# Performance work log

Measured on AMD Instinct MI355X. Metric: run time of the kernel, lower is better.

The kernel has to match this reference:

```python
import jax, jax.numpy as jnp
import numpy as np

N_NODES = 50000
N_EDGES = 800000
D_FEAT = 128
N_LAYERS = 3
HALF = 64  # units // 2 per kernel in tf_geometric MeanGraphSage
HIDDEN = 256
NUM_LABELS = 40


def setup_inputs() -> dict:
    key = jax.random.key(0)
    ks = jax.random.split(key, 6)
    x = jax.random.normal(ks[0], (N_NODES, D_FEAT), dtype=jnp.float32)
    edge_index = jax.random.randint(ks[1], (2, N_EDGES), 0, N_NODES, dtype=jnp.int32)
    self_kernels = jax.random.normal(ks[2], (N_LAYERS, D_FEAT, HALF), dtype=jnp.float32) * 0.05
    neighbor_kernels = jax.random.normal(ks[3], (N_LAYERS, D_FEAT, HALF), dtype=jnp.float32) * 0.05
    biases = jnp.zeros((N_LAYERS, 2 * HALF), dtype=jnp.float32)
    mlp_w1 = jax.random.normal(ks[4], (2 * HALF, HIDDEN), dtype=jnp.float32) * 0.05
    mlp_b1 = jnp.zeros((HIDDEN,), dtype=jnp.float32)
    mlp_w2 = jax.random.normal(ks[5], (HIDDEN, NUM_LABELS), dtype=jnp.float32) * 0.05
    mlp_b2 = jnp.zeros((NUM_LABELS,), dtype=jnp.float32)
    return {"x": x, "edge_index": edge_index, "self_kernels": self_kernels,
            "neighbor_kernels": neighbor_kernels, "biases": biases,
            "mlp_w1": mlp_w1, "mlp_b1": mlp_b1, "mlp_w2": mlp_w2, "mlp_b2": mlp_b2}


def reference(x, edge_index, self_kernels, neighbor_kernels, biases,
              mlp_w1, mlp_b1, mlp_w2, mlp_b2):
    n = x.shape[0]
    row, col = edge_index[0], edge_index[1]  # row: target node, col: source node
    # in-degree counts (graph is fixed across layers)
    ones = jnp.ones((edge_index.shape[1],), dtype=x.dtype)
    deg = jax.ops.segment_sum(ones, row, num_segments=n)  # [N]
    inv_deg = (1.0 / jnp.maximum(deg, 1.0))[:, None]      # [N,1]

    h = x
    for i in range(N_LAYERS):
        # mean-neighbor aggregation: gather source feats, segment-sum to targets
        nbr_sum = jax.ops.segment_sum(h[col], row, num_segments=n)  # [N,D]
        nbr_mean = nbr_sum * inv_deg
        from_self = h @ self_kernels[i]        # [N,HALF]
        from_nbr = nbr_mean @ neighbor_kernels[i]  # [N,HALF]
        h = jax.nn.relu(jnp.concatenate([from_self, from_nbr], axis=1) + biases[i])

    # MLP head (Flatten on [N,128] is a no-op)
    h = jax.nn.relu(h @ mlp_w1 + mlp_b1)
    return h @ mlp_w2 + mlp_b2
```

## Files before the change

kernel.cpp:

```cpp
#include <hip/hip_runtime.h>
#include <hip/hip_bf16.h>
#include <hip/hip_fp16.h>
#include <cstdint>
#include <cstddef>

#define N_NODES 50000
#define N_PAD   50176
#define N_EDGES 800000
#define D_FEAT  128
#define HALF    64
#define HIDDEN  256
#define LABELS  40

#define NBUCK 196
#define BCAP  5632
#define EDGES_PER_BLK 4096

#define HID_STRIDE 264

typedef __attribute__((ext_vector_type(8))) short bf16x8;
typedef __attribute__((ext_vector_type(4))) float f32x4;

#define PK_SELF(L) ((size_t)(L) * 8192)
#define PK_NBR(L)  (24576 + (size_t)(L) * 8192)
#define PK_W1      49152
#define PK_W2      81920
#define PK_TOTAL   94208

__device__ inline uint16_t f2bf_bits(float f) {
    __hip_bfloat16 b = __float2bfloat16(f);
    uint16_t u; __builtin_memcpy(&u, &b, 2); return u;
}

__device__ inline float2 h2f(uint32_t u) {
    __half2 h; __builtin_memcpy(&h, &u, 4);
    return __half22float2(h);
}

__global__ __launch_bounds__(1024) void bucket_scatter_kernel(
        const int* __restrict__ row, const int* __restrict__ col,
        int* __restrict__ bucket_cursor, uint32_t* __restrict__ staged) {
    __shared__ int hist[NBUCK];
    __shared__ int hbase[NBUCK];
    int tid  = threadIdx.x;
    int e0   = blockIdx.x * EDGES_PER_BLK;
    int eend = e0 + EDGES_PER_BLK; if (eend > N_EDGES) eend = N_EDGES;

    for (int i = tid; i < NBUCK; i += 1024) hist[i] = 0;
    __syncthreads();

    int rr[4], cc[4]; int ne = 0;
    for (int e = e0 + tid; e < eend; e += 1024) {
        rr[ne] = row[e]; cc[ne] = col[e]; ne++;
    }
    for (int i = 0; i < ne; i++) atomicAdd(&hist[rr[i] >> 8], 1);
    __syncthreads();

    for (int i = tid; i < NBUCK; i += 1024) {
        hbase[i] = atomicAdd(&bucket_cursor[i], hist[i]);
        hist[i]  = 0;
    }
    __syncthreads();

    for (int i = 0; i < ne; i++) {
        int b   = rr[i] >> 8;
        int off = atomicAdd(&hist[b], 1);
        int pos = hbase[b] + off;
        if (pos < BCAP)
            staged[(size_t)b * BCAP + pos] =
                ((uint32_t)(rr[i] & 255) << 16) | (uint32_t)cc[i];
    }
}

__global__ __launch_bounds__(256) void pack_all_kernel(
        const float* __restrict__ selfk, const float* __restrict__ nbrk,
        const float* __restrict__ w1, const float* __restrict__ w2,
        __hip_bfloat16* __restrict__ wpack) {
    int m = blockIdx.y;
    const float* W; int K, Ncols, Npad; size_t dstoff;
    if (m < 3)      { W = selfk + (size_t)m*D_FEAT*HALF;      K=128; Ncols=64;  Npad=64;  dstoff = PK_SELF(m); }
    else if (m < 6) { W = nbrk  + (size_t)(m-3)*D_FEAT*HALF;  K=128; Ncols=64;  Npad=64;  dstoff = PK_NBR(m-3); }
    else if (m == 6){ W = w1;                                 K=128; Ncols=256; Npad=256; dstoff = PK_W1; }
    else            { W = w2;                                 K=256; Ncols=40;  Npad=48;  dstoff = PK_W2; }
    int ksteps = K / 32;
    int total  = ksteps * (Npad / 16) * 64;
    int t = blockIdx.x * blockDim.x + threadIdx.x;
    if (t >= total) return;
    int lane = t & 63;
    int rest = t >> 6;
    int ks   = rest % ksteps;
    int ns   = rest / ksteps;
    int colb = ns * 16 + (lane & 15);
    int kb   = ks * 32 + (lane >> 4) * 8;
    __hip_bfloat16* dst = wpack + dstoff + (size_t)t * 8;
#pragma unroll
    for (int j = 0; j < 8; j++) {
        float v = (colb < Ncols) ? W[(size_t)(kb + j) * Ncols + colb] : 0.f;
        dst[j] = __float2bfloat16(v);
    }
}

template<bool AF32>
__device__ inline void gemm_wave_body(
        const void* __restrict__ Ain, int row0, int lane,
        const __hip_bfloat16* __restrict__ wpack_self,
        const __hip_bfloat16* __restrict__ wpack_nbr,
        const float* __restrict__ bias,
        __hip_bfloat16* __restrict__ hout, uint16_t* __restrict__ zn) {
    int lrow = lane & 15, lgrp = lane >> 4;

    const __hip_bfloat16 *hr0 = nullptr, *hr1 = nullptr;
    const float *xr0 = nullptr, *xr1 = nullptr;
    if constexpr (AF32) {
        const float* x = (const float*)Ain;
        int r0 = min(row0 + lrow, N_NODES - 1);
        int r1 = min(row0 + lrow + 16, N_NODES - 1);
        xr0 = x + (size_t)r0 * D_FEAT + lgrp * 8;
        xr1 = x + (size_t)r1 * D_FEAT + lgrp * 8;
    } else {
        const __hip_bfloat16* h = (const __hip_bfloat16*)Ain;
        hr0 = h + (size_t)(row0 + lrow) * D_FEAT + lgrp * 8;
        hr1 = hr0 + (size_t)16 * D_FEAT;
    }

    f32x4 accS[2][4] = {};
    f32x4 accN[2][4] = {};
#pragma unroll
    for (int ks = 0; ks < 4; ks++) {
        bf16x8 a0, a1;
        if constexpr (AF32) {
            float4 u0  = *(const float4*)(xr0 + ks * 32);
            float4 u0b = *(const float4*)(xr0 + ks * 32 + 4);
            float4 u1  = *(const float4*)(xr1 + ks * 32);
            float4 u1b = *(const float4*)(xr1 + ks * 32 + 4);
            float f0[8] = {u0.x, u0.y, u0.z, u0.w, u0b.x, u0b.y, u0b.z, u0b.w};
            float f1[8] = {u1.x, u1.y, u1.z, u1.w, u1b.x, u1b.y, u1b.z, u1b.w};
#pragma unroll
            for (int j = 0; j < 8; j++) { a0[j] = (short)f2bf_bits(f0[j]); a1[j] = (short)f2bf_bits(f1[j]); }
        } else {
            a0 = *(const bf16x8*)(hr0 + ks * 32);
            a1 = *(const bf16x8*)(hr1 + ks * 32);
        }
#pragma unroll
        for (int ns = 0; ns < 4; ns++) {
            bf16x8 bs = *(const bf16x8*)(wpack_self + ((size_t)(ns * 4 + ks) * 64 + lane) * 8);
            accS[0][ns] = __builtin_amdgcn_mfma_f32_16x16x32_bf16(a0, bs, accS[0][ns], 0, 0, 0);
            accS[1][ns] = __builtin_amdgcn_mfma_f32_16x16x32_bf16(a1, bs, accS[1][ns], 0, 0, 0);
            bf16x8 bn = *(const bf16x8*)(wpack_nbr + ((size_t)(ns * 4 + ks) * 64 + lane) * 8);
            accN[0][ns] = __builtin_amdgcn_mfma_f32_16x16x32_bf16(a0, bn, accN[0][ns], 0, 0, 0);
            accN[1][ns] = __builtin_amdgcn_mfma_f32_16x16x32_bf16(a1, bn, accN[1][ns], 0, 0, 0);
        }
    }
#pragma unroll
    for (int t = 0; t < 2; t++) {
#pragma unroll
        for (int ns = 0; ns < 4; ns++) {
            int colS = ns * 16 + lrow;
            float bvS = bias[colS];
#pragma unroll
            for (int i = 0; i < 4; i++) {
                int r = row0 + t * 16 + lgrp * 4 + i;
                hout[(size_t)r * D_FEAT + colS] =
                    __float2bfloat16(fmaxf(accS[t][ns][i] + bvS, 0.f));
                __half hz = __float2half(accN[t][ns][i]);
                uint16_t hb; __builtin_memcpy(&hb, &hz, 2);
                zn[(size_t)r * HALF + colS] = hb;
            }
        }
    }
}

__global__ __launch_bounds__(256, 2) void layer_gemm_kernel(
        const void* __restrict__ Ain,
        const __hip_bfloat16* __restrict__ wpack_self,
        const __hip_bfloat16* __restrict__ wpack_nbr,
        const float* __restrict__ bias,
        __hip_bfloat16* __restrict__ hout, uint16_t* __restrict__ zn) {
    int wave = threadIdx.x >> 6, lane = threadIdx.x & 63;
    int row0 = blockIdx.x * 128 + wave * 32;
    gemm_wave_body<false>(Ain, row0, lane, wpack_self, wpack_nbr, bias, hout, zn);
}

__global__ __launch_bounds__(512, 2) void gemm0_fill_kernel(
        const float* __restrict__ x,
        const __hip_bfloat16* __restrict__ wpack_self,
        const __hip_bfloat16* __restrict__ wpack_nbr,
        const float* __restrict__ bias,
        __hip_bfloat16* __restrict__ hout, uint16_t* __restrict__ zn,
        const uint32_t* __restrict__ staged, const int* __restrict__ bucket_cursor,
        int* __restrict__ deg, int* __restrict__ rowstart,
        float* __restrict__ inv_deg, uint16_t* __restrict__ csr_col) {
    __shared__ int cnt[256];
    __shared__ int excl[256];
    __shared__ int wt[4];
    __shared__ int seg[BCAP];
    __shared__ int base_s;

    if (blockIdx.x < 196) {
        int wave = threadIdx.x >> 6, lane = threadIdx.x & 63;
        int row0 = blockIdx.x * 256 + wave * 32;
        gemm_wave_body<true>((const void*)x, row0, lane,
                             wpack_self, wpack_nbr, bias, hout, zn);
        return;
    }

    int b   = blockIdx.x - 196;
    int tid = threadIdx.x;

    if (tid < 64) {
        int partial = 0;
        for (int i = tid; i < b; i += 64) partial += bucket_cursor[i];
#pragma unroll
        for (int off = 32; off > 0; off >>= 1)
            partial += __shfl_down(partial, off, 64);
        if (tid == 0) base_s = partial;
    }
    if (tid < 256) cnt[tid] = 0;
    __syncthreads();

    int total = bucket_cursor[b]; if (total > BCAP) total = BCAP;
    int gbase = base_s;
    const uint32_t* st = staged + (size_t)b * BCAP;

    for (int i = tid; i < total; i += 512) atomicAdd(&cnt[st[i] >> 16], 1);
    __syncthreads();

    int lane = tid & 63, wid = tid >> 6;
    int v = 0, s = 0;
    if (tid < 256) {
        v = cnt[tid]; s = v;
#pragma unroll
        for (int off = 1; off < 64; off <<= 1) {
            int t = __shfl_up(s, off, 64);
            if (lane >= off) s += t;
        }
        if (lane == 63) wt[wid] = s;
    }
    __syncthreads();
    if (tid == 0) { int a = 0; for (int i = 0; i < 4; i++) { int t = wt[i]; wt[i] = a; a += t; } }
    __syncthreads();
    if (tid < 256) {
        int ex = s - v + wt[wid];
        excl[tid] = ex;
        int node = (b << 8) + tid;
        if (node < N_NODES) {
            deg[node]      = v;
            rowstart[node] = gbase + ex;
            inv_deg[node]  = 1.0f / fmaxf((float)v, 1.0f);
        }
    }
    __syncthreads();
    for (int i = tid; i < total; i += 512) {
        uint32_t u = st[i];
        int p = atomicAdd(&excl[u >> 16], 1);
        seg[p] = (int)(u & 0xffffu);
    }
    __syncthreads();
    for (int i = tid; i < total; i += 512)
        csr_col[gbase + i] = (uint16_t)seg[i];
}

__global__ __launch_bounds__(128) void agg8_kernel(
        const uint16_t* __restrict__ zn, const uint16_t* __restrict__ csr_col,
        const int* __restrict__ rowstart, const int* __restrict__ deg,
        const float* __restrict__ inv_deg, const float* __restrict__ bias64,
        __hip_bfloat16* __restrict__ hout) {
    int gid  = blockIdx.x * 128 + threadIdx.x;
    int wnum = gid >> 6;
    int lane = threadIdx.x & 63;
    int sub  = lane >> 3;
    int sl   = lane & 7;
    int node = wnum * 8 + sub;
    int start = rowstart[node];
    int d     = deg[node];
    const uint32_t* zw = (const uint32_t*)zn;
    float acc[8] = {};

#define ACC8H(U) {                                                      \
    float2 t0 = h2f((U).x); acc[0] += t0.x; acc[1] += t0.y;             \
    float2 t1 = h2f((U).y); acc[2] += t1.x; acc[3] += t1.y;             \
    float2 t2 = h2f((U).z); acc[4] += t2.x; acc[5] += t2.y;             \
    float2 t3 = h2f((U).w); acc[6] += t3.x; acc[7] += t3.y; }

    if (d > 0) {
        int last = start + d - 1;
        int s[8];
#pragma unroll
        for (int k = 0; k < 8; k++) s[k] = csr_col[min(start + k, last)];
        int j = 0;
        for (; j + 8 <= d; j += 8) {
            int p[8];
#pragma unroll
            for (int k = 0; k < 8; k++) p[k] = csr_col[min(start + j + 8 + k, last)];
            uint4 u0 = *(const uint4*)(zw + (size_t)s[0] * 32 + sl * 4);
            uint4 u1 = *(const uint4*)(zw + (size_t)s[1] * 32 + sl * 4);
            uint4 u2 = *(const uint4*)(zw + (size_t)s[2] * 32 + sl * 4);
            uint4 u3 = *(const uint4*)(zw + (size_t)s[3] * 32 + sl * 4);
            uint4 u4 = *(const uint4*)(zw + (size_t)s[4] * 32 + sl * 4);
            uint4 u5 = *(const uint4*)(zw + (size_t)s[5] * 32 + sl * 4);
            uint4 u6 = *(const uint4*)(zw + (size_t)s[6] * 32 + sl * 4);
            uint4 u7 = *(const uint4*)(zw + (size_t)s[7] * 32 + sl * 4);
            ACC8H(u0); ACC8H(u1); ACC8H(u2); ACC8H(u3);
            ACC8H(u4); ACC8H(u5); ACC8H(u6); ACC8H(u7);
#pragma unroll
            for (int k = 0; k < 8; k++) s[k] = p[k];
        }
        int r = d - j;
#pragma unroll
        for (int k = 0; k < 8; k++) {
            if (k < r) {
                uint4 u = *(const uint4*)(zw + (size_t)s[k] * 32 + sl * 4);
                ACC8H(u);
            }
        }
    }
#undef ACC8H

    float inv = inv_deg[node];
    const float* bb = bias64 + sl * 8;
    float4 b0 = *(const float4*)bb;
    float4 b1 = *(const float4*)(bb + 4);
    uint4 p;
    p.x = (uint32_t)f2bf_bits(fmaxf(acc[0] * inv + b0.x, 0.f))
        | ((uint32_t)f2bf_bits(fmaxf(acc[1] * inv + b0.y, 0.f)) << 16);
    p.y = (uint32_t)f2bf_bits(fmaxf(acc[2] * inv + b0.z, 0.f))
        | ((uint32_t)f2bf_bits(fmaxf(acc[3] * inv + b0.w, 0.f)) << 16);
    p.z = (uint32_t)f2bf_bits(fmaxf(acc[4] * inv + b1.x, 0.f))
        | ((uint32_t)f2bf_bits(fmaxf(acc[5] * inv + b1.y, 0.f)) << 16);
    p.w = (uint32_t)f2bf_bits(fmaxf(acc[6] * inv + b1.z, 0.f))
        | ((uint32_t)f2bf_bits(fmaxf(acc[7] * inv + b1.w, 0.f)) << 16);
    *(uint4*)((uint32_t*)hout + (size_t)node * 64 + 32 + sl * 4) = p;
}

__global__ __launch_bounds__(256, 2) void mlp_fused_kernel(
        const __hip_bfloat16* __restrict__ h, const __hip_bfloat16* __restrict__ w1p,
        const float* __restrict__ b1, const __hip_bfloat16* __restrict__ w2p,
        const float* __restrict__ b2, float* __restrict__ out) {
    __shared__ __align__(16) uint16_t hid[128 * HID_STRIDE];
    int wave = threadIdx.x >> 6, lane = threadIdx.x & 63;
    int row0 = blockIdx.x * 128 + wave * 32;
    int lrow = lane & 15, lgrp = lane >> 4;

    {
        const __hip_bfloat16* ar0 = h + (size_t)(row0 + lrow) * D_FEAT + lgrp * 8;
        const __hip_bfloat16* ar1 = ar0 + (size_t)16 * D_FEAT;
        f32x4 acc[2][16] = {};
#pragma unroll 1
        for (int ks = 0; ks < 4; ks++) {
            bf16x8 a0 = *(const bf16x8*)(ar0 + ks * 32);
            bf16x8 a1 = *(const bf16x8*)(ar1 + ks * 32);
#pragma unroll
            for (int ns = 0; ns < 16; ns++) {
                bf16x8 bfr = *(const bf16x8*)(w1p + ((size_t)(ns * 4 + ks) * 64 + lane) * 8);
                acc[0][ns] = __builtin_amdgcn_mfma_f32_16x16x32_bf16(a0, bfr, acc[0][ns], 0, 0, 0);
                acc[1][ns] = __builtin_amdgcn_mfma_f32_16x16x32_bf16(a1, bfr, acc[1][ns], 0, 0, 0);
            }
        }
        int lbase = wave * 32;
#pragma unroll
        for (int t = 0; t < 2; t++) {
#pragma unroll
            for (int ns = 0; ns < 16; ns++) {
                int col = ns * 16 + lrow;
                float bv = b1[col];
#pragma unroll
                for (int i = 0; i < 4; i++) {
                    int lr = lbase + t * 16 + lgrp * 4 + i;
                    hid[lr * HID_STRIDE + col] =
                        f2bf_bits(fmaxf(acc[t][ns][i] + bv, 0.f));
                }
            }
        }
    }
    __syncthreads();

    const uint16_t* br0 = &hid[(wave * 32 + lrow) * HID_STRIDE + lgrp * 8];
    const uint16_t* br1 = br0 + 16 * HID_STRIDE;
    f32x4 acc2[2][3] = {};
#pragma unroll
    for (int ks = 0; ks < 8; ks++) {
        bf16x8 a0 = *(const bf16x8*)(br0 + ks * 32);
        bf16x8 a1 = *(const bf16x8*)(br1 + ks * 32);
#pragma unroll
        for (int ns = 0; ns < 3; ns++) {
            bf16x8 bfr = *(const bf16x8*)(w2p + ((size_t)(ns * 8 + ks) * 64 + lane) * 8);
            acc2[0][ns] = __builtin_amdgcn_mfma_f32_16x16x32_bf16(a0, bfr, acc2[0][ns], 0, 0, 0);
            acc2[1][ns] = __builtin_amdgcn_mfma_f32_16x16x32_bf16(a1, bfr, acc2[1][ns], 0, 0, 0);
        }
    }
#pragma unroll
    for (int t = 0; t < 2; t++) {
#pragma unroll
        for (int ns = 0; ns < 3; ns++) {
            int col = ns * 16 + lrow;
            if (col < LABELS) {
                float bv = b2[col];
#pragma unroll
                for (int i = 0; i < 4; i++) {
                    int r = row0 + t * 16 + lgrp * 4 + i;
                    if (r < N_NODES)
                        out[(size_t)r * LABELS + col] = acc2[t][ns][i] + bv;
                }
            }
        }
    }
}

extern "C" void kernel_launch(void* const* d_in, const int* in_sizes, int n_in,
                              void* d_out, int out_size, void* d_ws, size_t ws_size,
                              hipStream_t stream) {
    const float* x      = (const float*)d_in[0];
    const int*   ei     = (const int*)d_in[1];
    const float* selfk  = (const float*)d_in[2];
    const float* nbrk   = (const float*)d_in[3];
    const float* biases = (const float*)d_in[4];
    const float* w1     = (const float*)d_in[5];
    const float* b1     = (const float*)d_in[6];
    const float* w2     = (const float*)d_in[7];
    const float* b2     = (const float*)d_in[8];
    float* out = (float*)d_out;

    const int* row = ei;
    const int* col = ei + N_EDGES;

    char* ws = (char*)d_ws;
    size_t off = 0;
    auto alloc = [&](size_t bytes) -> char* {
        char* p = ws + off;
        off = (off + bytes + 255) & ~(size_t)255;
        return p;
    };
    int*   deg       = (int*)  alloc((size_t)N_NODES * 4);
    int*   rowstart  = (int*)  alloc((size_t)N_NODES * 4);
    float* inv_deg   = (float*)alloc((size_t)N_NODES * 4);
    int*   bucket_cursor = (int*)alloc(256 * 4);
    uint16_t* csr_col = (uint16_t*)alloc((size_t)N_EDGES * 2);
    uint32_t* staged = (uint32_t*)alloc((size_t)NBUCK * BCAP * 4);
    __hip_bfloat16* wpack  = (__hip_bfloat16*)alloc(PK_TOTAL * 2);
    __hip_bfloat16* hA     = (__hip_bfloat16*)alloc((size_t)N_PAD * D_FEAT * 2);
    __hip_bfloat16* hB     = (__hip_bfloat16*)alloc((size_t)N_PAD * D_FEAT * 2);
    uint16_t*       zn     = (uint16_t*)alloc((size_t)N_PAD * HALF * 2);

    hipMemsetAsync(bucket_cursor, 0, 256 * 4, stream);

    const int scat_blocks = (N_EDGES + EDGES_PER_BLK - 1) / EDGES_PER_BLK;
    bucket_scatter_kernel<<<scat_blocks, 1024, 0, stream>>>(row, col, bucket_cursor, staged);

    dim3 pgrid(16, 8);
    pack_all_kernel<<<pgrid, 256, 0, stream>>>(selfk, nbrk, w1, w2, wpack);

    const int layer_blocks = N_PAD / 128;
    const int agg_blocks   = N_NODES / 16;

    gemm0_fill_kernel<<<392, 512, 0, stream>>>(
        x, wpack + PK_SELF(0), wpack + PK_NBR(0), biases, hA, zn,
        staged, bucket_cursor, deg, rowstart, inv_deg, csr_col);
    agg8_kernel<<<agg_blocks, 128, 0, stream>>>(zn, csr_col, rowstart, deg,
                                                inv_deg, biases + 64, hA);
    layer_gemm_kernel<<<layer_blocks, 256, 0, stream>>>(
        (const void*)hA, wpack + PK_SELF(1), wpack + PK_NBR(1), biases + 128, hB, zn);
    agg8_kernel<<<agg_blocks, 128, 0, stream>>>(zn, csr_col, rowstart, deg,
                                                inv_deg, biases + 128 + 64, hB);
    layer_gemm_kernel<<<layer_blocks, 256, 0, stream>>>(
        (const void*)hB, wpack + PK_SELF(2), wpack + PK_NBR(2), biases + 256, hA, zn);
    agg8_kernel<<<agg_blocks, 128, 0, stream>>>(zn, csr_col, rowstart, deg,
                                                inv_deg, biases + 256 + 64, hA);

    mlp_fused_kernel<<<layer_blocks, 256, 0, stream>>>(hA, wpack + PK_W1, b1,
                                                       wpack + PK_W2, b2, out);
}
```

Baseline: 198.7 us.

## Fuse neighbor aggregation into next-layer GEMM and merge weight packing with scatter

Replaces the separate agg8 and layer_gemm kernels for layers 1-2 with a single agg_gemm kernel. It aggregates the neighbor half for a 128-row tile into LDS and immediately runs the MFMA GEMM, reading the self half from global. Because the aggregated neighbor half is never written back to global and re-read, zn is double-buffered to avoid read/write races across blocks. Weight packing is folded into the bucket scatter launch as extra blocks, which removes one kernel launch. The cost is a fused kernel with 4 gather passes per wave before the GEMM, and lower parallelism in the aggregation phase (392 blocks instead of 3125).

```diff
diff --git a/kernel.cpp b/kernel.cpp
--- a/kernel.cpp
+++ b/kernel.cpp
@@ -17,6 +17,7 @@
 #define EDGES_PER_BLK 4096
 
 #define HID_STRIDE 264
+#define NB_STRIDE  72
 
 typedef __attribute__((ext_vector_type(8))) short bf16x8;
 typedef __attribute__((ext_vector_type(4))) float f32x4;
@@ -37,9 +38,39 @@
     return __half22float2(h);
 }
 
-__global__ __launch_bounds__(1024) void bucket_scatter_kernel(
+__global__ __launch_bounds__(1024) void scatter_pack_kernel(
         const int* __restrict__ row, const int* __restrict__ col,
-        int* __restrict__ bucket_cursor, uint32_t* __restrict__ staged) {
+        int* __restrict__ bucket_cursor, uint32_t* __restrict__ staged,
+        const float* __restrict__ selfk, const float* __restrict__ nbrk,
+        const float* __restrict__ w1, const float* __restrict__ w2,
+        __hip_bfloat16* __restrict__ wpack) {
+    if (blockIdx.x >= 196) {
+        int pgid = (blockIdx.x - 196) * 1024 + threadIdx.x;
+        int m = pgid >> 12;
+        int t = pgid & 4095;
+        const float* W; int K, Ncols, Npad; size_t dstoff;
+        if (m < 3)      { W = selfk + (size_t)m*D_FEAT*HALF;      K=128; Ncols=64;  Npad=64;  dstoff = PK_SELF(m); }
+        else if (m < 6) { W = nbrk  + (size_t)(m-3)*D_FEAT*HALF;  K=128; Ncols=64;  Npad=64;  dstoff = PK_NBR(m-3); }
+        else if (m == 6){ W = w1;                                 K=128; Ncols=256; Npad=256; dstoff = PK_W1; }
+        else            { W = w2;                                 K=256; Ncols=40;  Npad=48;  dstoff = PK_W2; }
+        int ksteps = K / 32;
+        int total  = ksteps * (Npad / 16) * 64;
+        if (t >= total) return;
+        int lane = t & 63;
+        int rest = t >> 6;
+        int ks   = rest % ksteps;
+        int ns   = rest / ksteps;
+        int colb = ns * 16 + (lane & 15);
+        int kb   = ks * 32 + (lane >> 4) * 8;
+        __hip_bfloat16* dst = wpack + dstoff + (size_t)t * 8;
+#pragma unroll
+        for (int j = 0; j < 8; j++) {
+            float v = (colb < Ncols) ? W[(size_t)(kb + j) * Ncols + colb] : 0.f;
+            dst[j] = __float2bfloat16(v);
+        }
+        return;
+    }
+
     __shared__ int hist[NBUCK];
     __shared__ int hbase[NBUCK];
     int tid  = threadIdx.x;
@@ -69,34 +100,6 @@
         if (pos < BCAP)
             staged[(size_t)b * BCAP + pos] =
                 ((uint32_t)(rr[i] & 255) << 16) | (uint32_t)cc[i];
-    }
-}
-
-__global__ __launch_bounds__(256) void pack_all_kernel(
-        const float* __restrict__ selfk, const float* __restrict__ nbrk,
-        const float* __restrict__ w1, const float* __restrict__ w2,
-        __hip_bfloat16* __restrict__ wpack) {
-    int m = blockIdx.y;
-    const float* W; int K, Ncols, Npad; size_t dstoff;
-    if (m < 3)      { W = selfk + (size_t)m*D_FEAT*HALF;      K=128; Ncols=64;  Npad=64;  dstoff = PK_SELF(m); }
-    else if (m < 6) { W = nbrk  + (size_t)(m-3)*D_FEAT*HALF;  K=128; Ncols=64;  Npad=64;  dstoff = PK_NBR(m-3); }
-    else if (m == 6){ W = w1;                                 K=128; Ncols=256; Npad=256; dstoff = PK_W1; }
-    else            { W = w2;                                 K=256; Ncols=40;  Npad=48;  dstoff = PK_W2; }
-    int ksteps = K / 32;
-    int total  = ksteps * (Npad / 16) * 64;
-    int t = blockIdx.x * blockDim.x + threadIdx.x;
-    if (t >= total) return;
-    int lane = t & 63;
-    int rest = t >> 6;
-    int ks   = rest % ksteps;
-    int ns   = rest / ksteps;
-    int colb = ns * 16 + (lane & 15);
-    int kb   = ks * 32 + (lane >> 4) * 8;
-    __hip_bfloat16* dst = wpack + dstoff + (size_t)t * 8;
-#pragma unroll
-    for (int j = 0; j < 8; j++) {
-        float v = (colb < Ncols) ? W[(size_t)(kb + j) * Ncols + colb] : 0.f;
-        dst[j] = __float2bfloat16(v);
     }
 }
 
@@ -168,17 +171,6 @@
             }
         }
     }
-}
-
-__global__ __launch_bounds__(256, 2) void layer_gemm_kernel(
-        const void* __restrict__ Ain,
-        const __hip_bfloat16* __restrict__ wpack_self,
-        const __hip_bfloat16* __restrict__ wpack_nbr,
-        const float* __restrict__ bias,
-        __hip_bfloat16* __restrict__ hout, uint16_t* __restrict__ zn) {
-    int wave = threadIdx.x >> 6, lane = threadIdx.x & 63;
-    int row0 = blockIdx.x * 128 + wave * 32;
-    gemm_wave_body<false>(Ain, row0, lane, wpack_self, wpack_nbr, bias, hout, zn);
 }
 
 __global__ __launch_bounds__(512, 2) void gemm0_fill_kernel(
@@ -258,6 +250,135 @@
     __syncthreads();
     for (int i = tid; i < total; i += 512)
         csr_col[gbase + i] = (uint16_t)seg[i];
+}
+
+__global__ __launch_bounds__(256, 2) void agg_gemm_kernel(
+        const uint16_t* __restrict__ zn_in, const uint16_t* __restrict__ csr_col,
+        const int* __restrict__ rowstart, const int* __restrict__ deg,
+        const float* __restrict__ inv_deg, const float* __restrict__ bias_nbr,
+        const __hip_bfloat16* __restrict__ hself,
+        const __hip_bfloat16* __restrict__ wpack_self,
+        const __hip_bfloat16* __restrict__ wpack_nbr,
+        const float* __restrict__ bias_out,
+        __hip_bfloat16* __restrict__ hout, uint16_t* __restrict__ zn_out) {
+    __shared__ __align__(16) uint16_t nbr[128 * NB_STRIDE];
+    int wave = threadIdx.x >> 6, lane = threadIdx.x & 63;
+    int row0 = blockIdx.x * 128;
+
+    {
+        int sub = lane >> 3;
+        int sl  = lane & 7;
+        const uint32_t* zw = (const uint32_t*)zn_in;
+        const float* bb = bias_nbr + sl * 8;
+        float4 b0 = *(const float4*)bb;
+        float4 b1 = *(const float4*)(bb + 4);
+
+#define ACC8H(U) {                                                      \
+    float2 t0 = h2f((U).x); acc[0] += t0.x; acc[1] += t0.y;             \
+    float2 t1 = h2f((U).y); acc[2] += t1.x; acc[3] += t1.y;             \
+    float2 t2 = h2f((U).z); acc[4] += t2.x; acc[5] += t2.y;             \
+    float2 t3 = h2f((U).w); acc[6] += t3.x; acc[7] += t3.y; }
+
+        for (int it = 0; it < 4; it++) {
+            int nl   = it * 32 + wave * 8 + sub;
+            int node = min(row0 + nl, N_NODES - 1);
+            int start = rowstart[node];
+            int d     = deg[node];
+            float acc[8] = {};
+            if (d > 0) {
+                int last = start + d - 1;
+                int s[8];
+#pragma unroll
+                for (int k = 0; k < 8; k++) s[k] = csr_col[min(start + k, last)];
+                int j = 0;
+                for (; j + 8 <= d; j += 8) {
+                    int p[8];
+#pragma unroll
+                    for (int k = 0; k < 8; k++) p[k] = csr_col[min(start + j + 8 + k, last)];
+                    uint4 u0 = *(const uint4*)(zw + (size_t)s[0] * 32 + sl * 4);
+                    uint4 u1 = *(const uint4*)(zw + (size_t)s[1] * 32 + sl * 4);
+                    uint4 u2 = *(const uint4*)(zw + (size_t)s[2] * 32 + sl * 4);
+                    uint4 u3 = *(const uint4*)(zw + (size_t)s[3] * 32 + sl * 4);
+                    uint4 u4 = *(const uint4*)(zw + (size_t)s[4] * 32 + sl * 4);
+                    uint4 u5 = *(const uint4*)(zw + (size_t)s[5] * 32 + sl * 4);
+                    uint4 u6 = *(const uint4*)(zw + (size_t)s[6] * 32 + sl * 4);
+                    uint4 u7 = *(const uint4*)(zw + (size_t)s[7] * 32 + sl * 4);
+                    ACC8H(u0); ACC8H(u1); ACC8H(u2); ACC8H(u3);
+                    ACC8H(u4); ACC8H(u5); ACC8H(u6); ACC8H(u7);
+#pragma unroll
+                    for (int k = 0; k < 8; k++) s[k] = p[k];
+                }
+                int r = d - j;
+#pragma unroll
+                for (int k = 0; k < 8; k++) {
+                    if (k < r) {
+                        uint4 u = *(const uint4*)(zw + (size_t)s[k] * 32 + sl * 4);
+                        ACC8H(u);
+                    }
+                }
+            }
+            float inv = inv_deg[node];
+            uint4 p;
+            p.x = (uint32_t)f2bf_bits(fmaxf(acc[0] * inv + b0.x, 0.f))
+                | ((uint32_t)f2bf_bits(fmaxf(acc[1] * inv + b0.y, 0.f)) << 16);
+            p.y = (uint32_t)f2bf_bits(fmaxf(acc[2] * inv + b0.z, 0.f))
+                | ((uint32_t)f2bf_bits(fmaxf(acc[3] * inv + b0.w, 0.f)) << 16);
+            p.z = (uint32_t)f2bf_bits(fmaxf(acc[4] * inv + b1.x, 0.f))
+                | ((uint32_t)f2bf_bits(fmaxf(acc[5] * inv + b1.y, 0.f)) << 16);
+            p.w = (uint32_t)f2bf_bits(fmaxf(acc[6] * inv + b1.z, 0.f))
+                | ((uint32_t)f2bf_bits(fmaxf(acc[7] * inv + b1.w, 0.f)) << 16);
+            *(uint4*)&nbr[nl * NB_STRIDE + sl * 8] = p;
+        }
+#undef ACC8H
+    }
+    __syncthreads();
+
+    int lrow = lane & 15, lgrp = lane >> 4;
+    int rowb = row0 + wave * 32;
+    const __hip_bfloat16* hr0 = hself + (size_t)(rowb + lrow) * D_FEAT + lgrp * 8;
+    const __hip_bfloat16* hr1 = hr0 + (size_t)16 * D_FEAT;
+    const uint16_t* lr0 = &nbr[(wave * 32 + lrow) * NB_STRIDE + lgrp * 8];
+    const uint16_t* lr1 = lr0 + 16 * NB_STRIDE;
+
+    f32x4 accS[2][4] = {};
+    f32x4 accN[2][4] = {};
+#pragma unroll
+    for (int ks = 0; ks < 4; ks++) {
+        bf16x8 a0, a1;
+        if (ks < 2) {
+            a0 = *(const bf16x8*)(hr0 + ks * 32);
+            a1 = *(const bf16x8*)(hr1 + ks * 32);
+        } else {
+            a0 = *(const bf16x8*)(lr0 + (ks - 2) * 32);
+            a1 = *(const bf16x8*)(lr1 + (ks - 2) * 32);
+        }
+#pragma unroll
+        for (int ns = 0; ns < 4; ns++) {
+            bf16x8 bs = *(const bf16x8*)(wpack_self + ((size_t)(ns * 4 + ks) * 64 + lane) * 8);
+            accS[0][ns] = __builtin_amdgcn_mfma_f32_16x16x32_bf16(a0, bs, accS[0][ns], 0, 0, 0);
+            accS[1][ns] = __builtin_amdgcn_mfma_f32_16x16x32_bf16(a1, bs, accS[1][ns], 0, 0, 0);
+            bf16x8 bn = *(const bf16x8*)(wpack_nbr + ((size_t)(ns * 4 + ks) * 64 + lane) * 8);
+            accN[0][ns] = __builtin_amdgcn_mfma_f32_16x16x32_bf16(a0, bn, accN[0][ns], 0, 0, 0);
+            accN[1][ns] = __builtin_amdgcn_mfma_f32_16x16x32_bf16(a1, bn, accN[1][ns], 0, 0, 0);
+        }
+    }
+#pragma unroll
+    for (int t = 0; t < 2; t++) {
+#pragma unroll
+        for (int ns = 0; ns < 4; ns++) {
+            int colS = ns * 16 + lrow;
+            float bvS = bias_out[colS];
+#pragma unroll
+            for (int i = 0; i < 4; i++) {
+                int r = rowb + t * 16 + lgrp * 4 + i;
+                hout[(size_t)r * D_FEAT + colS] =
+                    __float2bfloat16(fmaxf(accS[t][ns][i] + bvS, 0.f));
+                __half hz = __float2half(accN[t][ns][i]);
+                uint16_t hb; __builtin_memcpy(&hb, &hz, 2);
+                zn_out[(size_t)r * HALF + colS] = hb;
+            }
+        }
+    }
 }
 
 __global__ __launch_bounds__(128) void agg8_kernel(
@@ -439,31 +560,30 @@
     __hip_bfloat16* wpack  = (__hip_bfloat16*)alloc(PK_TOTAL * 2);
     __hip_bfloat16* hA     = (__hip_bfloat16*)alloc((size_t)N_PAD * D_FEAT * 2);
     __hip_bfloat16* hB     = (__hip_bfloat16*)alloc((size_t)N_PAD * D_FEAT * 2);
-    uint16_t*       zn     = (uint16_t*)alloc((size_t)N_PAD * HALF * 2);
+    uint16_t*       znA    = (uint16_t*)alloc((size_t)N_PAD * HALF * 2);
+    uint16_t*       znB    = (uint16_t*)alloc((size_t)N_PAD * HALF * 2);
 
     hipMemsetAsync(bucket_cursor, 0, 256 * 4, stream);
 
-    const int scat_blocks = (N_EDGES + EDGES_PER_BLK - 1) / EDGES_PER_BLK;
-    bucket_scatter_kernel<<<scat_blocks, 1024, 0, stream>>>(row, col, bucket_cursor, staged);
-
-    dim3 pgrid(16, 8);
-    pack_all_kernel<<<pgrid, 256, 0, stream>>>(selfk, nbrk, w1, w2, wpack);
+    scatter_pack_kernel<<<228, 1024, 0, stream>>>(row, col, bucket_cursor, staged,
+                                                  selfk, nbrk, w1, w2, wpack);
 
     const int layer_blocks = N_PAD / 128;
     const int agg_blocks   = N_NODES / 16;
 
     gemm0_fill_kernel<<<392, 512, 0, stream>>>(
-        x, wpack + PK_SELF(0), wpack + PK_NBR(0), biases, hA, zn,
+        x, wpack + PK_SELF(0), wpack + PK_NBR(0), biases, hA, znA,
         staged, bucket_cursor, deg, rowstart, inv_deg, csr_col);
-    agg8_kernel<<<agg_blocks, 128, 0, stream>>>(zn, csr_col, rowstart, deg,
-                                                inv_deg, biases + 64, hA);
-    layer_gemm_kernel<<<layer_blocks, 256, 0, stream>>>(
-        (const void*)hA, wpack + PK_SELF(1), wpack + PK_NBR(1), biases + 128, hB, zn);
-    agg8_kernel<<<agg_blocks, 128, 0, stream>>>(zn, csr_col, rowstart, deg,
-                                                inv_deg, biases + 128 + 64, hB);
-    layer_gemm_kernel<<<layer_blocks, 256, 0, stream>>>(
-        (const void*)hB, wpack + PK_SELF(2), wpack + PK_NBR(2), biases + 256, hA, zn);
-    agg8_kernel<<<agg_blocks, 128, 0, stream>>>(zn, csr_col, rowstart, deg,
+
+    agg_gemm_kernel<<<layer_blocks, 256, 0, stream>>>(
+        znA, csr_col, rowstart, deg, inv_deg, biases + 64,
+        hA, wpack + PK_SELF(1), wpack + PK_NBR(1), biases + 128, hB, znB);
+
+    agg_gemm_kernel<<<layer_blocks, 256, 0, stream>>>(
+        znB, csr_col, rowstart, deg, inv_deg, biases + 128 + 64,
+        hB, wpack + PK_SELF(2), wpack + PK_NBR(2), biases + 256, hA, znA);
+
+    agg8_kernel<<<agg_blocks, 128, 0, stream>>>(znA, csr_col, rowstart, deg,
                                                 inv_deg, biases + 256 + 64, hA);
 
     mlp_fused_kernel<<<layer_blocks, 256, 0, stream>>>(hA, wpack + PK_W1, b1,
```

Measured after the change: 204.2 us. 1.03x slower.
